# Kernel optimization log

Measured on AMD Instinct MI355X. Metric: run time of the kernel, lower is better.

## Reference

```python
import jax, jax.numpy as jnp
import numpy as np

COMPRESSION = 2

def setup_inputs() -> dict:
    key = jax.random.key(0)
    k = jax.random.split(key, 5)
    B, H, W, C, Ci = 8, 56, 56, 256, 128
    return {
        "x": jax.random.normal(k[0], (B, H, W, C), dtype=jnp.float32),
        "w_theta": jax.random.normal(k[1], (C, Ci), dtype=jnp.float32) * (2.0 / C) ** 0.5,
        "w_phi": jax.random.normal(k[2], (C, Ci), dtype=jnp.float32) * (2.0 / C) ** 0.5,
        "w_g": jax.random.normal(k[3], (C, Ci), dtype=jnp.float32) * (2.0 / C) ** 0.5,
        "w_final": jax.random.normal(k[4], (Ci, C), dtype=jnp.float32) * (2.0 / Ci) ** 0.5,
    }

def _maxpool1d(z, pool):
    # z: [B, N, Ci]; non-overlapping max pool along N (Keras MaxPool1D default stride=pool)
    B, N, Ci = z.shape
    return z[:, : (N // pool) * pool].reshape(B, N // pool, pool, Ci).max(axis=2)

def reference(x, w_theta, w_phi, w_g, w_final):
    B, H, W, C = x.shape
    Ci = w_theta.shape[1]
    N = H * W
    xf = x.reshape(B, N, C)
    # 1x1 convs == per-position matmuls
    theta = xf @ w_theta                      # [B, N, Ci]
    phi = _maxpool1d(xf @ w_phi, COMPRESSION)  # [B, N/2, Ci]
    g = _maxpool1d(xf @ w_g, COMPRESSION)      # [B, N/2, Ci]
    f = jnp.einsum('bnc,bmc->bnm', theta, phi)  # [B, N, N/2]
    f = jax.nn.softmax(f, axis=-1)
    y = jnp.einsum('bnm,bmc->bnc', f, g)        # [B, N, Ci]
    z = y @ w_final                              # [B, N, C]
    return x + z.reshape(B, H, W, C)
```

## Files before the change

### kernel.cpp

```cpp
#include <hip/hip_runtime.h>

typedef _Float16 f16x8 __attribute__((ext_vector_type(8)));
typedef _Float16 f16x4 __attribute__((ext_vector_type(4)));
typedef short s16x4 __attribute__((ext_vector_type(4)));
typedef float f32x4 __attribute__((ext_vector_type(4)));

#define MFMA_K32(a, b, c) __builtin_amdgcn_mfma_f32_16x16x32_f16(a, b, c, 0, 0, 0)
#define MFMA_BF(a, b, c)  __builtin_amdgcn_mfma_f32_16x16x16bf16_1k(a, b, c, 0, 0, 0)
#define MFMA_F16(a, b, c) __builtin_amdgcn_mfma_f32_16x16x16f16(a, b, c, 0, 0, 0)


__device__ __forceinline__ f16x8 ld8f(const float* __restrict__ p) {
    f32x4 a = *(const f32x4*)p;
    f32x4 b = *(const f32x4*)(p + 4);
    f16x8 r;
    r[0] = (_Float16)a[0]; r[1] = (_Float16)a[1];
    r[2] = (_Float16)a[2]; r[3] = (_Float16)a[3];
    r[4] = (_Float16)b[0]; r[5] = (_Float16)b[1];
    r[6] = (_Float16)b[2]; r[7] = (_Float16)b[3];
    return r;
}
__device__ __forceinline__ unsigned f2bf_rne(float f) {
    unsigned u = __float_as_uint(f);
    return (u + 0x7FFFu + ((u >> 16) & 1u)) >> 16;
}
__device__ __forceinline__ int bfpack_rtz(float lo, float hi) {
    return (int)((__float_as_uint(hi) & 0xFFFF0000u) | (__float_as_uint(lo) >> 16));
}

__global__ __launch_bounds__(256) void k_prep(
    const float* __restrict__ wt, const float* __restrict__ wp,
    const float* __restrict__ wg, const float* __restrict__ wf,
    _Float16* __restrict__ wt_f, _Float16* __restrict__ wfT_f) {
    int i = blockIdx.x * 256 + threadIdx.x;
    if (i < 12288) {
        int w    = i >> 12;
        int rem  = i & 4095;
        int ctkc = rem >> 6;
        int l    = rem & 63;
        const float* src = (w == 0) ? wt : (w == 1) ? wp : wg;
        const float* s = src + ((ctkc & 7) * 32 + (l >> 4) * 8) * 128
                             + (ctkc >> 3) * 16 + (l & 15);
        f16x8 v;
#pragma unroll
        for (int jj = 0; jj < 8; ++jj) v[jj] = (_Float16)s[jj * 128];
        *(f16x8*)(wt_f + i * 8) = v;
    } else {
        int j    = i - 12288;
        int ct   = j >> 8;
        int rem  = j & 255;
        int qt   = rem >> 2;
        int kc2e = rem & 3;
        int col  = ct * 16 + (qt & 15);
        int qq   = qt >> 4;
        f16x8 v;
#pragma unroll
        for (int jp = 0; jp < 8; ++jp) {
            int Ci = (kc2e * 2 + (jp >> 2)) * 16 + qq * 4 + (jp & 3);
            v[jp] = (_Float16)wf[Ci * 256 + col];
        }
        *(f16x8*)(wfT_f + j * 8) = v;
    }
}

__global__ __launch_bounds__(256) void k_proj(
    const float* __restrict__ x,
    const _Float16* __restrict__ wt_f,
    _Float16* __restrict__ theta_f,
    _Float16* __restrict__ phi_f,
    short* __restrict__ g_f)
{
    const int u    = blockIdx.x * 4 + (threadIdx.x >> 6);
    const int lane = threadIdx.x & 63;
    const int q = lane >> 4, t = lane & 15;

    const int tt = u / 3;
    const int w  = u - tt * 3;

    const int mrow = tt * 16 + t;
    f16x8 af[8];
#pragma unroll
    for (int kc = 0; kc < 8; ++kc)
        af[kc] = ld8f(x + mrow * 256 + kc * 32 + q * 8);

    const f32x4 zero = {0.f, 0.f, 0.f, 0.f};
    f32x4 acc[8];
#pragma unroll
    for (int ct = 0; ct < 8; ++ct) acc[ct] = zero;

    if (w == 2) {
#pragma unroll
        for (int ct = 0; ct < 8; ++ct) {
            const _Float16* Wc = wt_f + ((w * 8 + ct) * 8) * 512 + lane * 8;
#pragma unroll
            for (int kc = 0; kc < 8; ++kc)
                acc[ct] = MFMA_K32(af[kc], *(const f16x8*)(Wc + kc * 512), acc[ct]);
        }
    } else {
#pragma unroll
        for (int ct = 0; ct < 8; ++ct) {
            const _Float16* Wc = wt_f + ((w * 8 + ct) * 8) * 512 + lane * 8;
#pragma unroll
            for (int kc = 0; kc < 8; ++kc)
                acc[ct] = MFMA_K32(*(const f16x8*)(Wc + kc * 512), af[kc], acc[ct]);
        }
    }

    if (w == 0) {
        _Float16* tb = theta_f + tt * 2048;
#pragma unroll
        for (int ct = 0; ct < 8; ++ct) {
            f16x4 v;
#pragma unroll
            for (int r = 0; r < 4; ++r) v[r] = (_Float16)acc[ct][r];
            const int off = (ct >> 1) * 512
                          + (((ct & 1) * 2 + (q >> 1)) * 16 + t) * 8 + 4 * (q & 1);
            *(f16x4*)(tb + off) = v;
        }
        return;
    }

    const int b     = tt / 196;
    const int tl    = tt - b * 196;
    const int chunk = tl >> 2;
    const int sub   = tl & 3;

    if (w == 1) {
        _Float16* pcb = phi_f + (b * 49 + chunk) * 4096;
#pragma unroll
        for (int ct = 0; ct < 8; ++ct) {
            f32x4 pm;
#pragma unroll
            for (int r = 0; r < 4; ++r)
                pm[r] = fmaxf(acc[ct][r], __shfl_xor(acc[ct][r], 1));
            if (!(t & 1)) {
                f16x4 v;
#pragma unroll
                for (int r = 0; r < 4; ++r) v[r] = (_Float16)pm[r];
                const int off = ((sub >> 1) * 4 + (ct >> 1)) * 512
                              + ((((ct & 1) * 2 + (q >> 1)) * 16)
                                 + (sub & 1) * 8 + (t >> 1)) * 8 + 4 * (q & 1);
                *(f16x4*)(pcb + off) = v;
            }
        }
    } else {
        const int h   = sub >> 1;
        short* gcb = g_f + (b * 49 + chunk) * 4096;
        const int qv  = (sub & 1) * 2 + (q >> 1);
        const int jj0 = (q & 1) * 2;
#pragma unroll
        for (int ct = 0; ct < 8; ++ct) {
            unsigned lo = f2bf_rne(fmaxf(acc[ct][0], acc[ct][1]));
            unsigned hi = f2bf_rne(fmaxf(acc[ct][2], acc[ct][3]));
            *(unsigned*)(gcb + ct * 512 + (qv * 16 + t) * 8 + h * 4 + jj0) = lo | (hi << 16);
        }
    }
}

__global__ __launch_bounds__(256) void k_attn(
    const _Float16* __restrict__ theta_f,
    const _Float16* __restrict__ phi_f,
    const short* __restrict__ g_f,
    const _Float16* __restrict__ wfT_f,
    const float* __restrict__ x,
    float* __restrict__ out)
{
    const int blk  = blockIdx.x;
    const int b    = blk & 7;
    const int blkm = blk >> 3;
    const int wave = threadIdx.x >> 6;
    const int lane = threadIdx.x & 63;
    const int q = lane >> 4, t = lane & 15;

    __shared__ __align__(16) _Float16 kv[2][8192];

    const int tIdx = b * 196 + blkm * 4 + wave;
    const _Float16* ph = phi_f + b * 200704;
    const _Float16* gt = (const _Float16*)(g_f + b * 200704);

    f16x8 qf[4];
#pragma unroll
    for (int kc = 0; kc < 4; ++kc)
        qf[kc] = *(const f16x8*)(theta_f + tIdx * 2048 + kc * 512 + lane * 8);

    const f32x4 zero = {0.f, 0.f, 0.f, 0.f};
    f32x4 o[8];
#pragma unroll
    for (int ct = 0; ct < 8; ++ct) o[ct] = zero;
    float lsum = 0.f;
    const float L2E = 1.44269504f, SHIFT = 104.0f;

    const _Float16* src0 = (wave < 2) ? (ph + wave * 2048) : (gt + (wave - 2) * 2048);
    const int doff = wave * 2048;

    f16x8 sr[4];
#pragma unroll
    for (int j = 0; j < 4; ++j)
        sr[j] = *(const f16x8*)(src0 + j * 512 + lane * 8);
#pragma unroll
    for (int j = 0; j < 4; ++j)
        *(f16x8*)(&kv[0][doff + j * 512 + lane * 8]) = sr[j];
    __syncthreads();

    for (int i = 0; i < 49; ++i) {
        if (i + 1 < 49) {
            const _Float16* s = src0 + (i + 1) * 4096;
#pragma unroll
            for (int j = 0; j < 4; ++j)
                sr[j] = *(const f16x8*)(s + j * 512 + lane * 8);
        }

        const _Float16* buf = &kv[i & 1][0];
        f32x4 st0 = zero, st1 = zero;
#pragma unroll
        for (int kc = 0; kc < 4; ++kc) {
            f16x8 a0 = *(const f16x8*)(buf + kc * 512 + lane * 8);
            f16x8 a1 = *(const f16x8*)(buf + (4 + kc) * 512 + lane * 8);
            st0 = MFMA_K32(a0, qf[kc], st0);
            st1 = MFMA_K32(a1, qf[kc], st1);
        }

        f32x4 p0, p1;
#pragma unroll
        for (int r = 0; r < 4; ++r) {
            p0[r] = exp2f(st0[r] * L2E - SHIFT);
            p1[r] = exp2f(st1[r] * L2E - SHIFT);
        }
        lsum += ((p0[0] + p0[1]) + (p0[2] + p0[3]))
              + ((p1[0] + p1[1]) + (p1[2] + p1[3]));
        union { int i2[2]; s16x4 v; } u0, u1;
        u0.i2[0] = bfpack_rtz(p0[0], p0[1]);
        u0.i2[1] = bfpack_rtz(p0[2], p0[3]);
        u1.i2[0] = bfpack_rtz(p1[0], p1[1]);
        u1.i2[1] = bfpack_rtz(p1[2], p1[3]);

#pragma unroll
        for (int ct = 0; ct < 8; ++ct) {
            union { f16x8 f; s16x4 s[2]; } uv;
            uv.f = *(const f16x8*)(buf + 4096 + ct * 512 + lane * 8);
            o[ct] = MFMA_BF(uv.s[0], u0.v, o[ct]);
            o[ct] = MFMA_BF(uv.s[1], u1.v, o[ct]);
        }

        if (i + 1 < 49) {
            _Float16* d = &kv[(i + 1) & 1][doff];
#pragma unroll
            for (int j = 0; j < 4; ++j)
                *(f16x8*)(d + j * 512 + lane * 8) = sr[j];
        }
        __syncthreads();
    }

    float lf = lsum;
    lf += __shfl_xor(lf, 16);
    lf += __shfl_xor(lf, 32);
    const float inv = 1.0f / lf;

    f16x4 yf[8];
#pragma unroll
    for (int ct = 0; ct < 8; ++ct)
#pragma unroll
        for (int r = 0; r < 4; ++r)
            yf[ct][r] = (_Float16)(o[ct][r] * inv);

    const int row = tIdx * 16 + t;
#pragma unroll 2
    for (int ctile = 0; ctile < 16; ++ctile) {
        union { f16x8 v8; f16x4 v4[2]; } w[4];
#pragma unroll
        for (int p = 0; p < 4; ++p)
            w[p].v8 = *(const f16x8*)(wfT_f + ctile * 2048 + lane * 32 + p * 8);
        f32x4 acc = zero;
#pragma unroll
        for (int kc2 = 0; kc2 < 8; ++kc2)
            acc = MFMA_F16(w[kc2 >> 1].v4[kc2 & 1], yf[kc2], acc);
        const int col = ctile * 16 + q * 4;
        f32x4 xv = *(const f32x4*)(x + row * 256 + col);
        *(f32x4*)(out + row * 256 + col) = acc + xv;
    }
}

extern "C" void kernel_launch(void* const* d_in, const int* in_sizes, int n_in,
                              void* d_out, int out_size, void* d_ws, size_t ws_size,
                              hipStream_t stream) {
    const float* x  = (const float*)d_in[0];
    const float* wt = (const float*)d_in[1];
    const float* wp = (const float*)d_in[2];
    const float* wg = (const float*)d_in[3];
    const float* wf = (const float*)d_in[4];
    float* out = (float*)d_out;

    _Float16* ws      = (_Float16*)d_ws;
    _Float16* wt_f    = ws;
    _Float16* wfT_f   = ws + 98304;
    _Float16* theta_f = ws + 131072;
    _Float16* phi_f   = ws + 3342336;
    short*    g_f     = (short*)(ws + 4947968);

    k_prep<<<dim3(64),   256, 0, stream>>>(wt, wp, wg, wf, wt_f, wfT_f);
    k_proj<<<dim3(1176), 256, 0, stream>>>(x, wt_f, theta_f, phi_f, g_f);
    k_attn<<<dim3(392),  256, 0, stream>>>(theta_f, phi_f, g_f, wfT_f, x, out);
}
```

Measured before the change: 161.1 us.

## Split attention waves over key halves with two query tiles each; stage projection weights in LDS

Each attention wave now handles two query tiles over half of the key block, so every K/V fragment read from LDS feeds two MFMAs. Partial outputs and softmax sums are then combined across wave pairs through shared memory. The g layout is changed to a 4-element-per-lane form to match the new V reads. The projection kernel switches to a 2D grid where each block loads one weight matrix into LDS and reuses it across four waves. The costs are extra register pressure, a cross-wave reduction with added barriers, and 64KB of LDS per projection block, which can limit occupancy.

Result: faster. 151.3 us (-6.1%).

```diff
diff --git a/kernel.cpp b/kernel.cpp
--- a/kernel.cpp
+++ b/kernel.cpp
@@ -70,12 +70,22 @@
     _Float16* __restrict__ phi_f,
     short* __restrict__ g_f)
 {
-    const int u    = blockIdx.x * 4 + (threadIdx.x >> 6);
+    const int w    = blockIdx.y;
+    const int wave = threadIdx.x >> 6;
     const int lane = threadIdx.x & 63;
     const int q = lane >> 4, t = lane & 15;
-
-    const int tt = u / 3;
-    const int w  = u - tt * 3;
+    const int tt = blockIdx.x * 4 + wave;
+
+    __shared__ __align__(16) _Float16 Wl[32768];
+    {
+        const _Float16* src = wt_f + w * 32768;
+#pragma unroll
+        for (int j = 0; j < 16; ++j) {
+            const int o8 = (j * 256 + threadIdx.x) * 8;
+            *(f16x8*)(Wl + o8) = *(const f16x8*)(src + o8);
+        }
+    }
+    __syncthreads();
 
     const int mrow = tt * 16 + t;
     f16x8 af[8];
@@ -91,7 +101,7 @@
     if (w == 2) {
 #pragma unroll
         for (int ct = 0; ct < 8; ++ct) {
-            const _Float16* Wc = wt_f + ((w * 8 + ct) * 8) * 512 + lane * 8;
+            const _Float16* Wc = Wl + (ct * 8) * 512 + lane * 8;
 #pragma unroll
             for (int kc = 0; kc < 8; ++kc)
                 acc[ct] = MFMA_K32(af[kc], *(const f16x8*)(Wc + kc * 512), acc[ct]);
@@ -99,7 +109,7 @@
     } else {
 #pragma unroll
         for (int ct = 0; ct < 8; ++ct) {
-            const _Float16* Wc = wt_f + ((w * 8 + ct) * 8) * 512 + lane * 8;
+            const _Float16* Wc = Wl + (ct * 8) * 512 + lane * 8;
 #pragma unroll
             for (int kc = 0; kc < 8; ++kc)
                 acc[ct] = MFMA_K32(*(const f16x8*)(Wc + kc * 512), af[kc], acc[ct]);
@@ -152,7 +162,7 @@
         for (int ct = 0; ct < 8; ++ct) {
             unsigned lo = f2bf_rne(fmaxf(acc[ct][0], acc[ct][1]));
             unsigned hi = f2bf_rne(fmaxf(acc[ct][2], acc[ct][3]));
-            *(unsigned*)(gcb + ct * 512 + (qv * 16 + t) * 8 + h * 4 + jj0) = lo | (hi << 16);
+            *(unsigned*)(gcb + (ct * 2 + h) * 256 + (qv * 16 + t) * 4 + jj0) = lo | (hi << 16);
         }
     }
 }
@@ -171,23 +181,30 @@
     const int wave = threadIdx.x >> 6;
     const int lane = threadIdx.x & 63;
     const int q = lane >> 4, t = lane & 15;
+    const int p = wave >> 1;
+    const int h = wave & 1;
 
     __shared__ __align__(16) _Float16 kv[2][8192];
-
-    const int tIdx = b * 196 + blkm * 4 + wave;
+    __shared__ float lred[2][2][64];
+
+    const int tIdx0 = b * 196 + blkm * 4;
     const _Float16* ph = phi_f + b * 200704;
     const _Float16* gt = (const _Float16*)(g_f + b * 200704);
 
-    f16x8 qf[4];
-#pragma unroll
-    for (int kc = 0; kc < 4; ++kc)
-        qf[kc] = *(const f16x8*)(theta_f + tIdx * 2048 + kc * 512 + lane * 8);
+    f16x8 qf[2][4];
+#pragma unroll
+    for (int m = 0; m < 2; ++m)
+#pragma unroll
+        for (int kc = 0; kc < 4; ++kc)
+            qf[m][kc] = *(const f16x8*)(theta_f + (tIdx0 + 2 * p + m) * 2048 + kc * 512 + lane * 8);
 
     const f32x4 zero = {0.f, 0.f, 0.f, 0.f};
-    f32x4 o[8];
-#pragma unroll
-    for (int ct = 0; ct < 8; ++ct) o[ct] = zero;
-    float lsum = 0.f;
+    f32x4 o[2][8];
+#pragma unroll
+    for (int m = 0; m < 2; ++m)
+#pragma unroll
+        for (int ct = 0; ct < 8; ++ct) o[m][ct] = zero;
+    float lsum[2] = {0.f, 0.f};
     const float L2E = 1.44269504f, SHIFT = 104.0f;
 
     const _Float16* src0 = (wave < 2) ? (ph + wave * 2048) : (gt + (wave - 2) * 2048);
@@ -202,6 +219,7 @@
         *(f16x8*)(&kv[0][doff + j * 512 + lane * 8]) = sr[j];
     __syncthreads();
 
+#pragma unroll 1
     for (int i = 0; i < 49; ++i) {
         if (i + 1 < 49) {
             const _Float16* s = src0 + (i + 1) * 4096;
@@ -211,35 +229,31 @@
         }
 
         const _Float16* buf = &kv[i & 1][0];
-        f32x4 st0 = zero, st1 = zero;
+        f32x4 st[2] = {zero, zero};
 #pragma unroll
         for (int kc = 0; kc < 4; ++kc) {
-            f16x8 a0 = *(const f16x8*)(buf + kc * 512 + lane * 8);
-            f16x8 a1 = *(const f16x8*)(buf + (4 + kc) * 512 + lane * 8);
-            st0 = MFMA_K32(a0, qf[kc], st0);
-            st1 = MFMA_K32(a1, qf[kc], st1);
-        }
-
-        f32x4 p0, p1;
-#pragma unroll
-        for (int r = 0; r < 4; ++r) {
-            p0[r] = exp2f(st0[r] * L2E - SHIFT);
-            p1[r] = exp2f(st1[r] * L2E - SHIFT);
-        }
-        lsum += ((p0[0] + p0[1]) + (p0[2] + p0[3]))
-              + ((p1[0] + p1[1]) + (p1[2] + p1[3]));
-        union { int i2[2]; s16x4 v; } u0, u1;
-        u0.i2[0] = bfpack_rtz(p0[0], p0[1]);
-        u0.i2[1] = bfpack_rtz(p0[2], p0[3]);
-        u1.i2[0] = bfpack_rtz(p1[0], p1[1]);
-        u1.i2[1] = bfpack_rtz(p1[2], p1[3]);
-
-#pragma unroll
-        for (int ct = 0; ct < 8; ++ct) {
-            union { f16x8 f; s16x4 s[2]; } uv;
-            uv.f = *(const f16x8*)(buf + 4096 + ct * 512 + lane * 8);
-            o[ct] = MFMA_BF(uv.s[0], u0.v, o[ct]);
-            o[ct] = MFMA_BF(uv.s[1], u1.v, o[ct]);
+            f16x8 a = *(const f16x8*)(buf + (h * 4 + kc) * 512 + lane * 8);
+            st[0] = MFMA_K32(a, qf[0][kc], st[0]);
+            st[1] = MFMA_K32(a, qf[1][kc], st[1]);
+        }
+
+        union { int i2[2]; s16x4 v; } u[2];
+#pragma unroll
+        for (int m = 0; m < 2; ++m) {
+            f32x4 pv;
+#pragma unroll
+            for (int r = 0; r < 4; ++r)
+                pv[r] = exp2f(st[m][r] * L2E - SHIFT);
+            lsum[m] += (pv[0] + pv[1]) + (pv[2] + pv[3]);
+            u[m].i2[0] = bfpack_rtz(pv[0], pv[1]);
+            u[m].i2[1] = bfpack_rtz(pv[2], pv[3]);
+        }
+
+#pragma unroll
+        for (int ct = 0; ct < 8; ++ct) {
+            s16x4 vf = *(const s16x4*)(buf + 4096 + (ct * 2 + h) * 256 + lane * 4);
+            o[0][ct] = MFMA_BF(vf, u[0].v, o[0][ct]);
+            o[1][ct] = MFMA_BF(vf, u[1].v, o[1][ct]);
         }
 
         if (i + 1 < 49) {
@@ -251,7 +265,49 @@
         __syncthreads();
     }
 
-    float lf = lsum;
+    float* cb = (float*)&kv[0][0];
+    if (h == 1) {
+#pragma unroll
+        for (int m = 0; m < 2; ++m) {
+#pragma unroll
+            for (int ct = 0; ct < 8; ++ct)
+                *(f32x4*)&cb[p * 4096 + (m * 8 + ct) * 256 + lane * 4] = o[m][ct];
+            lred[p][m][lane] = lsum[m];
+        }
+    }
+    __syncthreads();
+    if (h == 0) {
+#pragma unroll
+        for (int m = 0; m < 2; ++m) {
+#pragma unroll
+            for (int ct = 0; ct < 8; ++ct)
+                o[m][ct] += *(const f32x4*)&cb[p * 4096 + (m * 8 + ct) * 256 + lane * 4];
+            lsum[m] += lred[p][m][lane];
+        }
+    }
+    __syncthreads();
+    if (h == 0) {
+#pragma unroll
+        for (int ct = 0; ct < 8; ++ct)
+            *(f32x4*)&cb[p * 4096 + ct * 256 + lane * 4] = o[1][ct];
+        lred[p][0][lane] = lsum[1];
+    }
+    __syncthreads();
+
+    f32x4 ow[8];
+    float lw;
+    if (h == 0) {
+#pragma unroll
+        for (int ct = 0; ct < 8; ++ct) ow[ct] = o[0][ct];
+        lw = lsum[0];
+    } else {
+#pragma unroll
+        for (int ct = 0; ct < 8; ++ct)
+            ow[ct] = *(const f32x4*)&cb[p * 4096 + ct * 256 + lane * 4];
+        lw = lred[p][0][lane];
+    }
+
+    float lf = lw;
     lf += __shfl_xor(lf, 16);
     lf += __shfl_xor(lf, 32);
     const float inv = 1.0f / lf;
@@ -261,15 +317,15 @@
     for (int ct = 0; ct < 8; ++ct)
 #pragma unroll
         for (int r = 0; r < 4; ++r)
-            yf[ct][r] = (_Float16)(o[ct][r] * inv);
-
-    const int row = tIdx * 16 + t;
+            yf[ct][r] = (_Float16)(ow[ct][r] * inv);
+
+    const int row = (tIdx0 + 2 * p + h) * 16 + t;
 #pragma unroll 2
     for (int ctile = 0; ctile < 16; ++ctile) {
         union { f16x8 v8; f16x4 v4[2]; } w[4];
 #pragma unroll
-        for (int p = 0; p < 4; ++p)
-            w[p].v8 = *(const f16x8*)(wfT_f + ctile * 2048 + lane * 32 + p * 8);
+        for (int pp = 0; pp < 4; ++pp)
+            w[pp].v8 = *(const f16x8*)(wfT_f + ctile * 2048 + lane * 32 + pp * 8);
         f32x4 acc = zero;
 #pragma unroll
         for (int kc2 = 0; kc2 < 8; ++kc2)
@@ -297,7 +353,7 @@
     _Float16* phi_f   = ws + 3342336;
     short*    g_f     = (short*)(ws + 4947968);
 
-    k_prep<<<dim3(64),   256, 0, stream>>>(wt, wp, wg, wf, wt_f, wfT_f);
-    k_proj<<<dim3(1176), 256, 0, stream>>>(x, wt_f, theta_f, phi_f, g_f);
-    k_attn<<<dim3(392),  256, 0, stream>>>(theta_f, phi_f, g_f, wfT_f, x, out);
-}
+    k_prep<<<dim3(64),      256, 0, stream>>>(wt, wp, wg, wf, wt_f, wfT_f);
+    k_proj<<<dim3(392, 3),  256, 0, stream>>>(x, wt_f, theta_f, phi_f, g_f);
+    k_attn<<<dim3(392),     256, 0, stream>>>(theta_f, phi_f, g_f, wfT_f, x, out);
+}
```
